# Kernel tuning notes

Hardware: AMD Instinct MI355X
Metric: run time of the kernel (lower is better)

## Reference

```python
import math
import jax, jax.numpy as jnp
import numpy as np

# Model dims (from Weatherformer defaults: hidden = 8 heads * factor 8 = 64)
B, S, E, H, L = 8, 1024, 64, 8, 3
HD = E // H          # head_dim = 8
FF = 4 * E           # feedforward = 256
IN = 31              # input_dim (weather features)
OUT = 31             # output_dim
NG = 31              # granularity embedding table size
EPS = 1e-5


def setup_inputs() -> dict:
    key = jax.random.key(0)
    ks = jax.random.split(key, 12)
    p = lambda k, shape: jax.random.normal(k, shape, jnp.float32) * 0.05
    return {
        "weather": jax.random.normal(ks[0], (B, S, IN), jnp.float32),
        "coords": jax.random.uniform(ks[1], (B, 2), jnp.float32, -90.0, 90.0),
        "temporal_index": jax.random.randint(ks[2], (B, 2), 0, NG),
        "W_emb": p(ks[3], (IN, E)), "b_emb": jnp.zeros((E,), jnp.float32),
        "W_qkv": p(ks[4], (L, E, 3 * E)), "b_qkv": jnp.zeros((L, 3 * E), jnp.float32),
        "W_out": p(ks[5], (L, E, E)), "b_out": jnp.zeros((L, E), jnp.float32),
        "gran": p(ks[6], (L, NG, E)),
        "g1": jnp.ones((L, E), jnp.float32), "be1": jnp.zeros((L, E), jnp.float32),
        "W1": p(ks[7], (L, E, FF)), "b1": jnp.zeros((L, FF), jnp.float32),
        "W2": p(ks[8], (L, FF, E)), "b2": jnp.zeros((L, E), jnp.float32),
        "g2": jnp.ones((L, E), jnp.float32), "be2": jnp.zeros((L, E), jnp.float32),
        "W_fc": p(ks[9], (E, OUT)), "b_fc": jnp.zeros((OUT,), jnp.float32),
    }


def _layernorm(x, g, b):
    m = jnp.mean(x, axis=-1, keepdims=True)
    v = jnp.var(x, axis=-1, keepdims=True)
    return (x - m) / jnp.sqrt(v + EPS) * g + b


def _pos_encoding(coords):
    # div_term over every 4th channel: [E/4]
    div = jnp.exp(jnp.arange(0, E, 4, dtype=jnp.float32) * (-math.log(10000.0) / E))
    lat = coords[:, :1] / 180.0 * math.pi   # [B,1]
    lon = coords[:, 1:] / 180.0 * math.pi   # [B,1]
    tf = jnp.arange(S, dtype=jnp.float32)[:, None] * div          # [S, E/4]
    q = E // 4
    sin_tf = jnp.broadcast_to(jnp.sin(tf)[None], (B, S, q))       # channels 0::4
    cos_tf = jnp.broadcast_to(jnp.cos(tf)[None], (B, S, q))       # channels 1::4
    sin_lat = jnp.broadcast_to(jnp.sin(lat * div)[:, None, :], (B, S, q))  # 2::4
    cos_lon = jnp.broadcast_to(jnp.cos(lon * div)[:, None, :], (B, S, q))  # 3::4
    return jnp.stack([sin_tf, cos_tf, sin_lat, cos_lon], axis=-1).reshape(B, S, E)


def _attention(x, tg, W_qkv, b_qkv, W_out, b_out, gran_table):
    # Faithful replication of torch's (seq-major) qkv reshape quirk.
    qkv = x @ W_qkv + b_qkv                                  # [B,S,3E]
    qkv = qkv.reshape(B, S, 3, E).transpose(2, 0, 1, 3)      # [3,B,S,E]
    qkv = qkv.reshape(3, S, B * H, HD).transpose(0, 2, 1, 3) # [3,B*H,S,HD]
    q, k, v = qkv[0], qkv[1], qkv[2]
    ge = gran_table[tg].reshape(B * H, 1, HD)                # [B*H,1,HD]
    q = q + ge
    k = k + ge
    scores = jnp.einsum('bqd,bkd->bqk', q, k) * (HD ** -0.5) # [B*H,S,S]
    w = jax.nn.softmax(scores, axis=-1)                      # dropout = identity (eval)
    o = jnp.einsum('bqk,bkd->bqd', w, v)                     # [B*H,S,HD]
    o = o.transpose(1, 0, 2).reshape(B * S, E)
    return (o @ W_out + b_out).reshape(B, S, E)


def reference(weather, coords, temporal_index, W_emb, b_emb, W_qkv, b_qkv,
              W_out, b_out, gran, g1, be1, W1, b1, W2, b2, g2, be2, W_fc, b_fc):
    tg = temporal_index[:, 1:][:, :, None].astype(jnp.int32)  # [B,1,1]
    x = weather @ W_emb + b_emb                               # [B,S,E]
    x = x + _pos_encoding(coords)
    for l in range(L):
        a = _attention(x, tg, W_qkv[l], b_qkv[l], W_out[l], b_out[l], gran[l])
        x = _layernorm(x + a, g1[l], be1[l])
        ff = jax.nn.relu(x @ W1[l] + b1[l]) @ W2[l] + b2[l]
        x = _layernorm(x + ff, g2[l], be2[l])
    return x @ W_fc + b_fc                                    # [B,S,OUT]
```

## Files before the change

### kernel.cpp

```cpp
#include <hip/hip_runtime.h>
#include <math.h>

#define EPS 1e-5f

typedef float f32x16 __attribute__((ext_vector_type(16)));
typedef short short8 __attribute__((ext_vector_type(8)));

union U4S8 { uint4 u; short8 s; };

__device__ __forceinline__ float wave_sum64(float v) {
#pragma unroll
  for (int off = 32; off >= 1; off >>= 1) v += __shfl_xor(v, off, 64);
  return v;
}

__device__ __forceinline__ unsigned int bf16rne(float f) {
  unsigned int u = __float_as_uint(f);
  return (u + 0x7fffu + ((u >> 16) & 1u)) >> 16;
}
__device__ __forceinline__ unsigned int cvt_pk_bf16(float lo, float hi) {
  unsigned int r;
  asm("v_cvt_pk_bf16_f32 %0, %1, %2" : "=v"(r) : "v"(lo), "v"(hi));
  return r;
}

__global__ __launch_bounds__(192) void k_qkv0(
    const float* __restrict__ weather, const float* __restrict__ coords,
    const float* __restrict__ W_emb, const float* __restrict__ b_emb,
    const float* __restrict__ Wq, const float* __restrict__ bq,
    const float* __restrict__ gran, const int* __restrict__ tidx,
    float* __restrict__ x, unsigned int* __restrict__ qb,
    unsigned int* __restrict__ kbuf, unsigned short* __restrict__ vt) {
  int t = threadIdx.x;
  int row0 = blockIdx.x << 3;
  __shared__ float wrow[8][32];
  __shared__ float xs[8][64];
  for (int i = t; i < 256; i += 192) {
    int r = i >> 5, c2 = i & 31;
    if (c2 < 31) wrow[r][c2] = weather[(size_t)(row0 + r) * 31 + c2];
  }
  __syncthreads();
  int b = row0 >> 10;
  float lat = coords[b * 2 + 0] * 0.017453292519943295f;
  float lon = coords[b * 2 + 1] * 0.017453292519943295f;
  for (int idx = t; idx < 512; idx += 192) {
    int r = idx >> 6, e = idx & 63;
    int s = (row0 + r) & 1023;
    float acc = b_emb[e];
#pragma unroll
    for (int i = 0; i < 31; ++i) acc = fmaf(wrow[r][i], W_emb[i * 64 + e], acc);
    int g = e >> 2, rem = e & 3;
    float div = __expf(-0.5756462732485115f * (float)g);
    float pe;
    if (rem == 0)      pe = sinf((float)s * div);
    else if (rem == 1) pe = cosf((float)s * div);
    else if (rem == 2) pe = sinf(lat * div);
    else               pe = cosf(lon * div);
    float xv = acc + pe;
    xs[r][e] = xv;
    x[(size_t)(row0 + r) * 64 + e] = xv;
  }
  __syncthreads();
  float acc[8];
  float bias = bq[t];
#pragma unroll
  for (int r = 0; r < 8; ++r) acc[r] = bias;
#pragma unroll 4
  for (int k4 = 0; k4 < 16; ++k4) {
    float4 xv[8];
#pragma unroll
    for (int r = 0; r < 8; ++r) xv[r] = *(const float4*)(&xs[r][4 * k4]);
    float w0 = Wq[(4 * k4 + 0) * 192 + t];
    float w1 = Wq[(4 * k4 + 1) * 192 + t];
    float w2 = Wq[(4 * k4 + 2) * 192 + t];
    float w3 = Wq[(4 * k4 + 3) * 192 + t];
#pragma unroll
    for (int r = 0; r < 8; ++r) {
      acc[r] = fmaf(xv[r].x, w0, acc[r]);
      acc[r] = fmaf(xv[r].y, w1, acc[r]);
      acc[r] = fmaf(xv[r].z, w2, acc[r]);
      acc[r] = fmaf(xv[r].w, w3, acc[r]);
    }
  }
  int cq = t & 63;
  int hh = cq >> 3, hd = t & 7;
  int shi = (row0 & 1023) >> 3;
  int s2 = (b << 7) | shi;
  const float scl = 0.35355339059327373f;
#pragma unroll
  for (int r = 0; r < 8; ++r) {
    float o = acc[r];
    if (t < 128) o += gran[tidx[2 * r + 1] * 64 + cq];
    int bh = (r << 3) | hh;
    if (t < 64) {
      o *= scl;
      float nb = __shfl_down(o, 1, 64);
      if ((hd & 1) == 0)
        qb[((((size_t)bh << 10) | s2) << 2) + (hd >> 1)] =
            bf16rne(o) | (bf16rne(nb) << 16);
    } else if (t < 128) {
      float nb = __shfl_down(o, 1, 64);
      if ((hd & 1) == 0)
        kbuf[((((size_t)bh << 10) | s2) << 2) + (hd >> 1)] =
            bf16rne(o) | (bf16rne(nb) << 16);
    } else {
      vt[((size_t)bh << 13) + (hd << 10) + s2] = (unsigned short)bf16rne(o);
    }
  }
}

__global__ __launch_bounds__(512, 2) void k_attn(
    const unsigned int* __restrict__ qb, const unsigned int* __restrict__ kbuf,
    const unsigned short* __restrict__ vt, float* __restrict__ ao) {
  int bh = blockIdx.x >> 3, chunk = blockIdx.x & 7;
  int slo = bh >> 3, h = bh & 7;
  int t = threadIdx.x;
  int l = t & 63, w = t >> 6;
  int grp = w >> 1, kh = w & 1;
  int lq = l & 31, g = l >> 5;
  bool kl = (l < 32);
  bool vl = (lq < 8);
  int q = (chunk << 7) + (grp << 5) + lq;

  U4S8 qf;
  qf.u = make_uint4(0, 0, 0, 0);
  if (kl) qf.u = *(const uint4*)(qb + ((((size_t)bh << 10) + q) << 2));

  const uint4* kp = (const uint4*)(kbuf + ((size_t)bh << 12));
  const unsigned short* vp = vt + ((size_t)bh << 13);

  f32x16 O, Z;
#pragma unroll
  for (int i = 0; i < 16; ++i) { O[i] = 0.f; Z[i] = 0.f; }
  float m = -1e30f, ls = 0.f;

  int kb0 = kh << 4;
  for (int kblk = kb0; kblk < kb0 + 16; ++kblk) {
    U4S8 af;
    af.u = make_uint4(0, 0, 0, 0);
    if (kl) af.u = kp[(kblk << 5) + lq];
    f32x16 S = __builtin_amdgcn_mfma_f32_32x32x16_bf16(af.s, qf.s, Z, 0, 0, 0);

    float mx = S[0];
#pragma unroll
    for (int i = 1; i < 16; ++i) mx = fmaxf(mx, S[i]);
    mx = fmaxf(mx, __shfl_xor(mx, 32, 64));
    if (mx > m + 8.f) {
      float esc = __expf(m - mx);
      ls *= esc;
      O *= esc;
      m = mx;
    }
    float p[16];
#pragma unroll
    for (int i = 0; i < 16; ++i) p[i] = __expf(S[i] - m);
    float s01 = (p[0] + p[1]) + (p[2] + p[3]);
    float s23 = (p[4] + p[5]) + (p[6] + p[7]);
    float s45 = (p[8] + p[9]) + (p[10] + p[11]);
    float s67 = (p[12] + p[13]) + (p[14] + p[15]);
    ls += (s01 + s23) + (s45 + s67);

    unsigned va = cvt_pk_bf16(p[0], p[1]),  vb = cvt_pk_bf16(p[2], p[3]);
    unsigned vc = cvt_pk_bf16(p[4], p[5]),  vd = cvt_pk_bf16(p[6], p[7]);
    unsigned ve = cvt_pk_bf16(p[8], p[9]),  vf = cvt_pk_bf16(p[10], p[11]);
    unsigned vg = cvt_pk_bf16(p[12], p[13]), vh = cvt_pk_bf16(p[14], p[15]);
    unsigned sa = __shfl_xor((int)va, 32, 64), sb = __shfl_xor((int)vb, 32, 64);
    unsigned sc = __shfl_xor((int)vc, 32, 64), sd = __shfl_xor((int)vd, 32, 64);
    unsigned se = __shfl_xor((int)ve, 32, 64), sf = __shfl_xor((int)vf, 32, 64);
    unsigned sg = __shfl_xor((int)vg, 32, 64), sh = __shfl_xor((int)vh, 32, 64);
    U4S8 b1, b2;
    b1.u.x = kl ? va : sc;  b1.u.y = kl ? vb : sd;
    b1.u.z = kl ? sa : vc;  b1.u.w = kl ? sb : vd;
    b2.u.x = kl ? ve : sg;  b2.u.y = kl ? vf : sh;
    b2.u.z = kl ? se : vg;  b2.u.w = kl ? sf : vh;

    U4S8 v1, v2;
    v1.u = make_uint4(0, 0, 0, 0);
    v2.u = make_uint4(0, 0, 0, 0);
    if (vl) {
      const unsigned short* vb8 = vp + (lq << 10) + (kblk << 5) + (g << 3);
      v1.u = *(const uint4*)vb8;
      v2.u = *(const uint4*)(vb8 + 16);
    }
    O = __builtin_amdgcn_mfma_f32_32x32x16_bf16(v1.s, b1.s, O, 0, 0, 0);
    O = __builtin_amdgcn_mfma_f32_32x32x16_bf16(v2.s, b2.s, O, 0, 0, 0);
  }

  ls += __shfl_xor(ls, 32, 64);

  __shared__ float pm[4][64], pl[4][64];
  __shared__ float po[4][64][4];
  if (kh == 0) {
    pm[grp][l] = m;
    pl[grp][l] = ls;
    *(float4*)(&po[grp][l][0]) = make_float4(O[0], O[1], O[2], O[3]);
  }
  __syncthreads();
  if (kh == 1) {
    float mA = pm[grp][l], lsA = pl[grp][l];
    float nm = fmaxf(m, mA);
    float wB = __expf(m - nm), wA = __expf(mA - nm);
    float4 oA = *(const float4*)(&po[grp][l][0]);
    float inv = 1.0f / (ls * wB + lsA * wA);
    int bq2 = q >> 7, sq = ((q & 127) << 3) | slo;
    float* op = ao + (((size_t)((bq2 << 10) | sq)) << 6) + (h << 3) + (g << 2);
    *(float4*)op = make_float4((O[0] * wB + oA.x * wA) * inv,
                               (O[1] * wB + oA.y * wA) * inv,
                               (O[2] * wB + oA.z * wA) * inv,
                               (O[3] * wB + oA.w * wA) * inv);
  }
}

template <bool EMIT>
__global__ __launch_bounds__(512, 2) void k_fused(
    const float* x_in, const float* __restrict__ ao,
    const float* __restrict__ Wo, const float* __restrict__ bo,
    const float* __restrict__ g1, const float* __restrict__ be1,
    const float* __restrict__ W1, const float* __restrict__ b1,
    const float* __restrict__ W2, const float* __restrict__ b2,
    const float* __restrict__ g2, const float* __restrict__ be2,
    const float* __restrict__ Wq, const float* __restrict__ bq,
    const float* __restrict__ gran, const int* __restrict__ tidx,
    unsigned int* __restrict__ qbo, unsigned int* __restrict__ kbo,
    unsigned short* __restrict__ vto, float* __restrict__ x_out) {
  int t = threadIdx.x, w = t >> 6, c = t & 63;
  int ws = w << 1;
  int row_base = blockIdx.x << 4;
  int row0 = row_base + ws;
  __shared__ unsigned int w2b[8192];
  __shared__ float aos[16][64];
  __shared__ float x1s[16][64];
  __shared__ float h1s[16][256];
  for (int i = t; i < 8192; i += 512) {
    float2 f = *(const float2*)(W2 + 2 * i);
    w2b[i] = bf16rne(f.x) | (bf16rne(f.y) << 16);
  }
  float xin[2];
#pragma unroll
  for (int r = 0; r < 2; ++r) {
    aos[ws + r][c] = ao[(size_t)(row0 + r) * 64 + c];
    xin[r] = x_in[(size_t)(row0 + r) * 64 + c];
  }
  float acc[2];
  float bov = bo[c];
#pragma unroll
  for (int r = 0; r < 2; ++r) acc[r] = bov;
#pragma unroll 4
  for (int k4 = 0; k4 < 16; ++k4) {
    float w0 = Wo[(4 * k4 + 0) * 64 + c], w1 = Wo[(4 * k4 + 1) * 64 + c];
    float w2 = Wo[(4 * k4 + 2) * 64 + c], w3 = Wo[(4 * k4 + 3) * 64 + c];
#pragma unroll
    for (int r = 0; r < 2; ++r) {
      float4 av = *(const float4*)(&aos[ws + r][4 * k4]);
      acc[r] = fmaf(av.x, w0, acc[r]);
      acc[r] = fmaf(av.y, w1, acc[r]);
      acc[r] = fmaf(av.z, w2, acc[r]);
      acc[r] = fmaf(av.w, w3, acc[r]);
    }
  }
  float g1v = g1[c], be1v = be1[c];
  float x1v[2];
#pragma unroll
  for (int r = 0; r < 2; ++r) {
    float y = acc[r] + xin[r];
    float s1 = wave_sum64(y), s2 = wave_sum64(y * y);
    float mean = s1 * 0.015625f, var = s2 * 0.015625f - mean * mean;
    x1v[r] = (y - mean) * rsqrtf(var + EPS) * g1v + be1v;
    x1s[ws + r][c] = x1v[r];
  }
  float4 h[2];
  float4 b1v = *(const float4*)(b1 + 4 * c);
#pragma unroll
  for (int r = 0; r < 2; ++r) h[r] = b1v;
#pragma unroll 4
  for (int k4 = 0; k4 < 16; ++k4) {
    float4 w0 = *(const float4*)(W1 + (size_t)(4 * k4 + 0) * 256 + 4 * c);
    float4 w1 = *(const float4*)(W1 + (size_t)(4 * k4 + 1) * 256 + 4 * c);
    float4 w2 = *(const float4*)(W1 + (size_t)(4 * k4 + 2) * 256 + 4 * c);
    float4 w3 = *(const float4*)(W1 + (size_t)(4 * k4 + 3) * 256 + 4 * c);
#pragma unroll
    for (int r = 0; r < 2; ++r) {
      float4 xv = *(const float4*)(&x1s[ws + r][4 * k4]);
      h[r].x = fmaf(xv.x, w0.x, h[r].x); h[r].y = fmaf(xv.x, w0.y, h[r].y);
      h[r].z = fmaf(xv.x, w0.z, h[r].z); h[r].w = fmaf(xv.x, w0.w, h[r].w);
      h[r].x = fmaf(xv.y, w1.x, h[r].x); h[r].y = fmaf(xv.y, w1.y, h[r].y);
      h[r].z = fmaf(xv.y, w1.z, h[r].z); h[r].w = fmaf(xv.y, w1.w, h[r].w);
      h[r].x = fmaf(xv.z, w2.x, h[r].x); h[r].y = fmaf(xv.z, w2.y, h[r].y);
      h[r].z = fmaf(xv.z, w2.z, h[r].z); h[r].w = fmaf(xv.z, w2.w, h[r].w);
      h[r].x = fmaf(xv.w, w3.x, h[r].x); h[r].y = fmaf(xv.w, w3.y, h[r].y);
      h[r].z = fmaf(xv.w, w3.z, h[r].z); h[r].w = fmaf(xv.w, w3.w, h[r].w);
    }
  }
#pragma unroll
  for (int r = 0; r < 2; ++r) {
    h[r].x = fmaxf(h[r].x, 0.f); h[r].y = fmaxf(h[r].y, 0.f);
    h[r].z = fmaxf(h[r].z, 0.f); h[r].w = fmaxf(h[r].w, 0.f);
    *(float4*)(&h1s[ws + r][4 * c]) = h[r];
  }
  __syncthreads();
  int sh = (c & 1) ? 0 : 16;
  int wb2 = c >> 1;
  float acc2[2];
  float b2v = b2[c];
#pragma unroll
  for (int r = 0; r < 2; ++r) acc2[r] = b2v;
#pragma unroll 4
  for (int k4 = 0; k4 < 64; ++k4) {
    float w0 = __uint_as_float((w2b[(4 * k4 + 0) * 32 + wb2] << sh) & 0xffff0000u);
    float w1 = __uint_as_float((w2b[(4 * k4 + 1) * 32 + wb2] << sh) & 0xffff0000u);
    float w2 = __uint_as_float((w2b[(4 * k4 + 2) * 32 + wb2] << sh) & 0xffff0000u);
    float w3 = __uint_as_float((w2b[(4 * k4 + 3) * 32 + wb2] << sh) & 0xffff0000u);
#pragma unroll
    for (int r = 0; r < 2; ++r) {
      float4 hv = *(const float4*)(&h1s[ws + r][4 * k4]);
      acc2[r] = fmaf(hv.x, w0, acc2[r]);
      acc2[r] = fmaf(hv.y, w1, acc2[r]);
      acc2[r] = fmaf(hv.z, w2, acc2[r]);
      acc2[r] = fmaf(hv.w, w3, acc2[r]);
    }
  }
  float g2v = g2[c], be2v = be2[c];
#pragma unroll
  for (int r = 0; r < 2; ++r) {
    float y2 = acc2[r] + x1v[r];
    float t1 = wave_sum64(y2), t2 = wave_sum64(y2 * y2);
    float mean2 = t1 * 0.015625f, var2 = t2 * 0.015625f - mean2 * mean2;
    float xo = (y2 - mean2) * rsqrtf(var2 + EPS) * g2v + be2v;
    x_out[(size_t)(row0 + r) * 64 + c] = xo;
    aos[ws + r][c] = xo;
  }
  if (EMIT) {
    __syncthreads();
    bool gA = (t < 192), gB = (t >= 256 && t < 448);
    if (gA || gB) {
      int col = gA ? t : (t - 256);
      int rbase = gA ? 0 : 8;
      float qa[8];
      float bias = bq[col];
#pragma unroll
      for (int r = 0; r < 8; ++r) qa[r] = bias;
#pragma unroll 4
      for (int k4 = 0; k4 < 16; ++k4) {
        float w0 = Wq[(4 * k4 + 0) * 192 + col];
        float w1 = Wq[(4 * k4 + 1) * 192 + col];
        float w2v = Wq[(4 * k4 + 2) * 192 + col];
        float w3 = Wq[(4 * k4 + 3) * 192 + col];
#pragma unroll
        for (int r = 0; r < 8; ++r) {
          float4 av = *(const float4*)(&aos[rbase + r][4 * k4]);
          qa[r] = fmaf(av.x, w0, qa[r]);
          qa[r] = fmaf(av.y, w1, qa[r]);
          qa[r] = fmaf(av.z, w2v, qa[r]);
          qa[r] = fmaf(av.w, w3, qa[r]);
        }
      }
      int cq = col & 63, hh = cq >> 3, hd = col & 7;
      int bb = row_base >> 10;
      const float scl = 0.35355339059327373f;
#pragma unroll
      for (int r = 0; r < 8; ++r) {
        int rr = rbase + r;
        float o = qa[r];
        if (col < 128) o += gran[tidx[2 * (rr & 7) + 1] * 64 + cq];
        int row = row_base + rr;
        int s2 = (bb << 7) | ((row & 1023) >> 3);
        int bh = ((rr & 7) << 3) | hh;
        size_t base = ((size_t)(bh << 10)) | s2;
        if (col < 64) {
          o *= scl;
          float nb = __shfl_down(o, 1, 64);
          if ((hd & 1) == 0)
            qbo[(base << 2) + (hd >> 1)] = bf16rne(o) | (bf16rne(nb) << 16);
        } else if (col < 128) {
          float nb = __shfl_down(o, 1, 64);
          if ((hd & 1) == 0)
            kbo[(base << 2) + (hd >> 1)] = bf16rne(o) | (bf16rne(nb) << 16);
        } else {
          vto[((size_t)bh << 13) + (hd << 10) + s2] = (unsigned short)bf16rne(o);
        }
      }
    }
  }
}

__global__ __launch_bounds__(256) void k_head(
    const float* __restrict__ x, const float* __restrict__ Wfc,
    const float* __restrict__ bfc, float* __restrict__ out) {
  int gid = blockIdx.x * 256 + threadIdx.x;
  int r = gid >> 5, o = gid & 31;
  if (o >= 31) return;
  float acc = bfc[o];
  const float* xr = x + (size_t)r * 64;
#pragma unroll
  for (int i = 0; i < 64; ++i) acc = fmaf(xr[i], Wfc[i * 31 + o], acc);
  out[(size_t)r * 31 + o] = acc;
}

extern "C" void kernel_launch(void* const* d_in, const int* in_sizes, int n_in,
                              void* d_out, int out_size, void* d_ws, size_t ws_size,
                              hipStream_t stream) {
  const float* weather = (const float*)d_in[0];
  const float* coords  = (const float*)d_in[1];
  const int*   tidx    = (const int*)d_in[2];
  const float* W_emb   = (const float*)d_in[3];
  const float* b_emb   = (const float*)d_in[4];
  const float* W_qkv   = (const float*)d_in[5];
  const float* b_qkv   = (const float*)d_in[6];
  const float* W_out   = (const float*)d_in[7];
  const float* b_out   = (const float*)d_in[8];
  const float* gran    = (const float*)d_in[9];
  const float* g1      = (const float*)d_in[10];
  const float* be1     = (const float*)d_in[11];
  const float* W1      = (const float*)d_in[12];
  const float* b1      = (const float*)d_in[13];
  const float* W2      = (const float*)d_in[14];
  const float* b2      = (const float*)d_in[15];
  const float* g2      = (const float*)d_in[16];
  const float* be2     = (const float*)d_in[17];
  const float* W_fc    = (const float*)d_in[18];
  const float* b_fc    = (const float*)d_in[19];
  float* out = (float*)d_out;

  float* x = (float*)d_ws;
  unsigned int* qbw = (unsigned int*)(x + 8192 * 64);
  unsigned int* kbw = qbw + 64 * 1024 * 4;
  unsigned short* vtw = (unsigned short*)(kbw + 64 * 1024 * 4);
  float* ao = (float*)(vtw + 64 * 8 * 1024);

  k_qkv0<<<1024, 192, 0, stream>>>(weather, coords, W_emb, b_emb,
                                   W_qkv, b_qkv, gran, tidx,
                                   x, qbw, kbw, vtw);
  for (int l = 0; l < 3; ++l) {
    k_attn<<<512, 512, 0, stream>>>(qbw, kbw, vtw, ao);
    if (l < 2) {
      k_fused<true><<<512, 512, 0, stream>>>(
          x, ao, W_out + l * 64 * 64, b_out + l * 64,
          g1 + l * 64, be1 + l * 64, W1 + l * 64 * 256, b1 + l * 256,
          W2 + l * 256 * 64, b2 + l * 64, g2 + l * 64, be2 + l * 64,
          W_qkv + (l + 1) * 64 * 192, b_qkv + (l + 1) * 192,
          gran + (l + 1) * 31 * 64, tidx, qbw, kbw, vtw, x);
    } else {
      k_fused<false><<<512, 512, 0, stream>>>(
          x, ao, W_out + l * 64 * 64, b_out + l * 64,
          g1 + l * 64, be1 + l * 64, W1 + l * 64 * 256, b1 + l * 256,
          W2 + l * 256 * 64, b2 + l * 64, g2 + l * 64, be2 + l * 64,
          nullptr, nullptr, nullptr, nullptr, nullptr, nullptr, nullptr, x);
    }
  }
  k_head<<<1024, 256, 0, stream>>>(x, W_fc, b_fc, out);
}
```

Measured before the change: 181.9 us.

## Shrink fused FFN block to 8 rows, drop LDS bf16 W2 staging

```diff
diff --git a/kernel.cpp b/kernel.cpp
--- a/kernel.cpp
+++ b/kernel.cpp
@@ -212,7 +212,7 @@
 }
 
 template <bool EMIT>
-__global__ __launch_bounds__(512, 2) void k_fused(
+__global__ __launch_bounds__(256, 8) void k_fused(
     const float* x_in, const float* __restrict__ ao,
     const float* __restrict__ Wo, const float* __restrict__ bo,
     const float* __restrict__ g1, const float* __restrict__ be1,
@@ -225,16 +225,10 @@
     unsigned short* __restrict__ vto, float* __restrict__ x_out) {
   int t = threadIdx.x, w = t >> 6, c = t & 63;
   int ws = w << 1;
-  int row_base = blockIdx.x << 4;
+  int row_base = blockIdx.x << 3;
   int row0 = row_base + ws;
-  __shared__ unsigned int w2b[8192];
-  __shared__ float aos[16][64];
-  __shared__ float x1s[16][64];
-  __shared__ float h1s[16][256];
-  for (int i = t; i < 8192; i += 512) {
-    float2 f = *(const float2*)(W2 + 2 * i);
-    w2b[i] = bf16rne(f.x) | (bf16rne(f.y) << 16);
-  }
+  __shared__ float aos[8][64];
+  __shared__ float h1s[8][256];
   float xin[2];
 #pragma unroll
   for (int r = 0; r < 2; ++r) {
@@ -266,7 +260,7 @@
     float s1 = wave_sum64(y), s2 = wave_sum64(y * y);
     float mean = s1 * 0.015625f, var = s2 * 0.015625f - mean * mean;
     x1v[r] = (y - mean) * rsqrtf(var + EPS) * g1v + be1v;
-    x1s[ws + r][c] = x1v[r];
+    aos[ws + r][c] = x1v[r];
   }
   float4 h[2];
   float4 b1v = *(const float4*)(b1 + 4 * c);
@@ -280,7 +274,7 @@
     float4 w3 = *(const float4*)(W1 + (size_t)(4 * k4 + 3) * 256 + 4 * c);
 #pragma unroll
     for (int r = 0; r < 2; ++r) {
-      float4 xv = *(const float4*)(&x1s[ws + r][4 * k4]);
+      float4 xv = *(const float4*)(&aos[ws + r][4 * k4]);
       h[r].x = fmaf(xv.x, w0.x, h[r].x); h[r].y = fmaf(xv.x, w0.y, h[r].y);
       h[r].z = fmaf(xv.x, w0.z, h[r].z); h[r].w = fmaf(xv.x, w0.w, h[r].w);
       h[r].x = fmaf(xv.y, w1.x, h[r].x); h[r].y = fmaf(xv.y, w1.y, h[r].y);
@@ -297,19 +291,16 @@
     h[r].z = fmaxf(h[r].z, 0.f); h[r].w = fmaxf(h[r].w, 0.f);
     *(float4*)(&h1s[ws + r][4 * c]) = h[r];
   }
-  __syncthreads();
-  int sh = (c & 1) ? 0 : 16;
-  int wb2 = c >> 1;
   float acc2[2];
   float b2v = b2[c];
 #pragma unroll
   for (int r = 0; r < 2; ++r) acc2[r] = b2v;
 #pragma unroll 4
   for (int k4 = 0; k4 < 64; ++k4) {
-    float w0 = __uint_as_float((w2b[(4 * k4 + 0) * 32 + wb2] << sh) & 0xffff0000u);
-    float w1 = __uint_as_float((w2b[(4 * k4 + 1) * 32 + wb2] << sh) & 0xffff0000u);
-    float w2 = __uint_as_float((w2b[(4 * k4 + 2) * 32 + wb2] << sh) & 0xffff0000u);
-    float w3 = __uint_as_float((w2b[(4 * k4 + 3) * 32 + wb2] << sh) & 0xffff0000u);
+    float w0 = W2[(size_t)(4 * k4 + 0) * 64 + c];
+    float w1 = W2[(size_t)(4 * k4 + 1) * 64 + c];
+    float w2 = W2[(size_t)(4 * k4 + 2) * 64 + c];
+    float w3 = W2[(size_t)(4 * k4 + 3) * 64 + c];
 #pragma unroll
     for (int r = 0; r < 2; ++r) {
       float4 hv = *(const float4*)(&h1s[ws + r][4 * k4]);
@@ -331,47 +322,42 @@
   }
   if (EMIT) {
     __syncthreads();
-    bool gA = (t < 192), gB = (t >= 256 && t < 448);
-    if (gA || gB) {
-      int col = gA ? t : (t - 256);
-      int rbase = gA ? 0 : 8;
+    if (t < 192) {
       float qa[8];
-      float bias = bq[col];
+      float bias = bq[t];
 #pragma unroll
       for (int r = 0; r < 8; ++r) qa[r] = bias;
 #pragma unroll 4
       for (int k4 = 0; k4 < 16; ++k4) {
-        float w0 = Wq[(4 * k4 + 0) * 192 + col];
-        float w1 = Wq[(4 * k4 + 1) * 192 + col];
-        float w2v = Wq[(4 * k4 + 2) * 192 + col];
-        float w3 = Wq[(4 * k4 + 3) * 192 + col];
+        float w0 = Wq[(4 * k4 + 0) * 192 + t];
+        float w1 = Wq[(4 * k4 + 1) * 192 + t];
+        float w2v = Wq[(4 * k4 + 2) * 192 + t];
+        float w3 = Wq[(4 * k4 + 3) * 192 + t];
 #pragma unroll
         for (int r = 0; r < 8; ++r) {
-          float4 av = *(const float4*)(&aos[rbase + r][4 * k4]);
+          float4 av = *(const float4*)(&aos[r][4 * k4]);
           qa[r] = fmaf(av.x, w0, qa[r]);
           qa[r] = fmaf(av.y, w1, qa[r]);
           qa[r] = fmaf(av.z, w2v, qa[r]);
           qa[r] = fmaf(av.w, w3, qa[r]);
         }
       }
-      int cq = col & 63, hh = cq >> 3, hd = col & 7;
+      int cq = t & 63, hh = cq >> 3, hd = t & 7;
       int bb = row_base >> 10;
+      int s2 = (bb << 7) | ((row_base & 1023) >> 3);
       const float scl = 0.35355339059327373f;
 #pragma unroll
       for (int r = 0; r < 8; ++r) {
-        int rr = rbase + r;
         float o = qa[r];
-        if (col < 128) o += gran[tidx[2 * (rr & 7) + 1] * 64 + cq];
-        int row = row_base + rr;
-        int s2 = (bb << 7) | ((row & 1023) >> 3);
-        int bh = ((rr & 7) << 3) | hh;
+        if (t < 128) o += gran[tidx[2 * r + 1] * 64 + cq];
+        int bh = (r << 3) | hh;
         size_t base = ((size_t)(bh << 10)) | s2;
-        if (col < 64) {
+        if (t < 64) {
           o *= scl;
           float nb = __shfl_down(o, 1, 64);
           if ((hd & 1) == 0)
             qbo[(base << 2) + (hd >> 1)] = bf16rne(o) | (bf16rne(nb) << 16);
-        } else if (col < 128) {
+        } else if (t < 128) {
           float nb = __shfl_down(o, 1, 64);
           if ((hd & 1) == 0)
             kbo[(base << 2) + (hd >> 1)] = bf16rne(o) | (bf16rne(nb) << 16);
@@ -433,14 +419,14 @@
   for (int l = 0; l < 3; ++l) {
     k_attn<<<512, 512, 0, stream>>>(qbw, kbw, vtw, ao);
     if (l < 2) {
-      k_fused<true><<<512, 512, 0, stream>>>(
+      k_fused<true><<<1024, 256, 0, stream>>>(
           x, ao, W_out + l * 64 * 64, b_out + l * 64,
           g1 + l * 64, be1 + l * 64, W1 + l * 64 * 256, b1 + l * 256,
           W2 + l * 256 * 64, b2 + l * 64, g2 + l * 64, be2 + l * 64,
           W_qkv + (l + 1) * 64 * 192, b_qkv + (l + 1) * 192,
           gran + (l + 1) * 31 * 64, tidx, qbw, kbw, vtw, x);
     } else {
-      k_fused<false><<<512, 512, 0, stream>>>(
+      k_fused<false><<<1024, 256, 0, stream>>>(
           x, ao, W_out + l * 64 * 64, b_out + l * 64,
           g1 + l * 64, be1 + l * 64, W1 + l * 64 * 256, b1 + l * 256,
           W2 + l * 256 * 64, b2 + l * 64, g2 + l * 64, be2 + l * 64,
```

Result: slower. 201.7 us (+10.9%).
